# Kernel tuning notes

Measured on AMD Instinct MI355X. Metric: run time of the kernel, lower is better.

## Reference

```python
import jax, jax.numpy as jnp
import numpy as np

N_NODES = 50000
N_EDGES = 800000
IN_FEATS = 128
OUT_FEATS = 128
HEADS = 2
EW_DIMS = 2
NEG_SLOPE = 0.2


def setup_inputs() -> dict:
    key = jax.random.key(0)
    ks = jax.random.split(key, 8)
    feat = jax.random.normal(ks[0], (N_NODES, IN_FEATS), dtype=jnp.float32)
    e_w = jax.random.uniform(ks[1], (N_EDGES, EW_DIMS), dtype=jnp.float32)
    src = jax.random.randint(ks[2], (N_EDGES,), 0, N_NODES)
    dst = jax.random.randint(ks[3], (N_EDGES,), 0, N_NODES)
    # Learned params: per-head fc weight, attn vectors (xavier-ish scale)
    s = 1.0 / np.sqrt(IN_FEATS)
    W = jax.random.normal(ks[4], (HEADS, OUT_FEATS, IN_FEATS), dtype=jnp.float32) * s
    attn_l = jax.random.normal(ks[5], (HEADS, OUT_FEATS), dtype=jnp.float32) * s
    attn_r = jax.random.normal(ks[6], (HEADS, OUT_FEATS), dtype=jnp.float32) * s
    attn_ew = jax.random.normal(ks[7], (HEADS, EW_DIMS), dtype=jnp.float32)
    return {"feat": feat, "e_w": e_w, "src": src, "dst": dst,
            "W": W, "attn_l": attn_l, "attn_r": attn_r, "attn_ew": attn_ew}


def reference(feat, e_w, src, dst, W, attn_l, attn_r, attn_ew):
    N = feat.shape[0]
    # per-head projection: [N, H, O]
    ft = jnp.einsum('nf,hof->nho', feat, W)
    el = jnp.einsum('nho,ho->nh', ft, attn_l)           # [N, H]
    er = jnp.einsum('nho,ho->nh', ft, attn_r)           # [N, H]
    ew = jnp.einsum('ed,hd->eh', e_w, attn_ew)          # [E, H]
    # u_add_v + edge-weight attention + leaky_relu
    e = jax.nn.leaky_relu(el[src] + er[dst] + ew, NEG_SLOPE)  # [E, H]
    # edge_softmax grouped by destination node (numerically stable)
    emax = jax.ops.segment_max(e, dst, num_segments=N)
    emax = jnp.where(jnp.isfinite(emax), emax, 0.0)
    ee = jnp.exp(e - emax[dst])
    denom = jax.ops.segment_sum(ee, dst, num_segments=N)
    a = ee / jnp.where(denom[dst] > 0, denom[dst], 1.0)       # [E, H]
    # u_mul_e / sum aggregation: [N, H, O]
    m = ft[src] * a[:, :, None]
    rst = jax.ops.segment_sum(m, dst, num_segments=N)
    # residual (Identity since in_feats == out_feats) + elu, then cat heads
    rst = jax.nn.elu(rst + feat[:, None, :])
    return rst.reshape(N, -1)
```

## Files before the change

kernel.cpp:

```cpp
#include <hip/hip_runtime.h>
#include <hip/hip_bf16.h>
#include <math.h>

#define NNODES 50000
#define NEDGES 800000
#define INF 128
#define OUTF 128
#define HEADS 2
#define NEG_SLOPE 0.2f

#define CAP 32
#define OVFCAP 32768

__device__ __forceinline__ unsigned short f2bf(float f) {
    unsigned u = __float_as_uint(f);
    unsigned r = (u + 0x7FFFu + ((u >> 16) & 1u)) >> 16;
    return (unsigned short)r;
}
__device__ __forceinline__ float bf2f(unsigned short b) {
    return __uint_as_float((unsigned)b << 16);
}

typedef __attribute__((ext_vector_type(8))) short frag_ab;
typedef __attribute__((ext_vector_type(4))) float frag_cd;
struct us8 { ushort4 a, b; };

#define APITCH 136
#define EPITCH 68

__global__ __launch_bounds__(256) void prep(const float* __restrict__ W,
                                            const float* __restrict__ attn_l,
                                            const float* __restrict__ attn_r,
                                            int* cursor, int* ovfcnt,
                                            unsigned short* __restrict__ Wb,
                                            float* __restrict__ wl, float* __restrict__ wr,
                                            int N) {
    const int b = blockIdx.x, t = threadIdx.x;
    const int i = b * 256 + t;
    if (i < N) cursor[i] = 0;
    if (i == 0) *ovfcnt = 0;
    if (b < 32) {
        int idx = b * 256 + t;
        float4 g = *(const float4*)(W + (size_t)idx * 4);
        ushort4 v; v.x = f2bf(g.x); v.y = f2bf(g.y); v.z = f2bf(g.z); v.w = f2bf(g.w);
        *(ushort4*)(Wb + (size_t)idx * 4) = v;
    } else if (b == 32) {
        int h = t >> 7, f = t & 127;
        float s = 0.f;
#pragma unroll 8
        for (int o = 0; o < 128; ++o)
            s += attn_l[h * 128 + o] * W[(size_t)(h * 128 + o) * 128 + f];
        wl[t] = s;
    } else if (b == 33) {
        int h = t >> 7, f = t & 127;
        float s = 0.f;
#pragma unroll 8
        for (int o = 0; o < 128; ++o)
            s += attn_r[h * 128 + o] * W[(size_t)(h * 128 + o) * 128 + f];
        wr[t] = s;
    }
}

__global__ __launch_bounds__(256) void gemm_mfma(const float* __restrict__ feat,
                                                 const unsigned short* __restrict__ Wb,
                                                 unsigned short* __restrict__ ftb,
                                                 int N) {
    __shared__ unsigned short Asl[64 * APITCH];
    __shared__ unsigned short Bsl[64 * APITCH];
    const int t = threadIdx.x;
    const int n0 = blockIdx.x * 64;
    const int w = t >> 6, lane = t & 63;
    const int m16 = lane & 15, quad = lane >> 4;

#pragma unroll
    for (int i = 0; i < 8; ++i) {
        int q = t + i * 256;
        int r = q >> 5;
        int c4 = q & 31;
        int gn = n0 + r;
        float4 g = (gn < N) ? *(const float4*)(feat + (size_t)gn * INF + c4 * 4)
                            : make_float4(0.f, 0.f, 0.f, 0.f);
        ushort4 v; v.x = f2bf(g.x); v.y = f2bf(g.y); v.z = f2bf(g.z); v.w = f2bf(g.w);
        *(ushort4*)(&Asl[r * APITCH + c4 * 4]) = v;
    }

    const int arow = w * 16 + m16;

    for (int jt = 0; jt < 4; ++jt) {
        __syncthreads();
#pragma unroll
        for (int i = 0; i < 4; ++i) {
            int q = t + i * 256;
            int r = q >> 4;
            int c8 = q & 15;
            us8 v = *(const us8*)(Wb + (size_t)(jt * 64 + r) * 128 + c8 * 8);
            *(us8*)(&Bsl[r * APITCH + c8 * 8]) = v;
        }
        __syncthreads();

        frag_cd acc[4];
#pragma unroll
        for (int nt = 0; nt < 4; ++nt) acc[nt] = frag_cd{0.f, 0.f, 0.f, 0.f};

#pragma unroll
        for (int kc = 0; kc < 4; ++kc) {
            frag_ab af = *(frag_ab*)(&Asl[arow * APITCH + kc * 32 + quad * 8]);
#pragma unroll
            for (int nt = 0; nt < 4; ++nt) {
                frag_ab bf = *(frag_ab*)(&Bsl[(nt * 16 + m16) * APITCH + kc * 32 + quad * 8]);
                acc[nt] = __builtin_amdgcn_mfma_f32_16x16x32_bf16(af, bf, acc[nt], 0, 0, 0);
            }
        }

        __syncthreads();
        unsigned short* ep = &Bsl[w * 16 * EPITCH];
#pragma unroll
        for (int nt = 0; nt < 4; ++nt) {
#pragma unroll
            for (int reg = 0; reg < 4; ++reg)
                ep[(quad * 4 + reg) * EPITCH + nt * 16 + m16] = f2bf(acc[nt][reg]);
        }
        int r = lane >> 2;
        int c = lane & 3;
        us8 v0 = *(us8*)(&ep[r * EPITCH + c * 16]);
        us8 v1 = *(us8*)(&ep[r * EPITCH + c * 16 + 8]);
        int gm = n0 + w * 16 + r;
        if (gm < N) {
            *(us8*)(ftb + (size_t)gm * 256 + jt * 64 + c * 16) = v0;
            *(us8*)(ftb + (size_t)gm * 256 + jt * 64 + c * 16 + 8) = v1;
        }
    }
}

__global__ __launch_bounds__(256) void eler_kernel(const float* __restrict__ feat,
                                                   const float* __restrict__ wl,
                                                   const float* __restrict__ wr,
                                                   float2* __restrict__ el,
                                                   float2* __restrict__ er, int N) {
    __shared__ float swl[256], swr[256];
    const int t = threadIdx.x;
    swl[t] = wl[t];
    swr[t] = wr[t];
    __syncthreads();
    const int w = t >> 6, lane = t & 63;
    const int n = blockIdx.x * 4 + w;
    if (n >= N) return;
    float2 f = *(const float2*)(feat + (size_t)n * INF + lane * 2);
    float l0 = f.x * swl[lane * 2] + f.y * swl[lane * 2 + 1];
    float l1 = f.x * swl[128 + lane * 2] + f.y * swl[128 + lane * 2 + 1];
    float r0 = f.x * swr[lane * 2] + f.y * swr[lane * 2 + 1];
    float r1 = f.x * swr[128 + lane * 2] + f.y * swr[128 + lane * 2 + 1];
#pragma unroll
    for (int m = 1; m < 64; m <<= 1) {
        l0 += __shfl_xor(l0, m, 64);
        l1 += __shfl_xor(l1, m, 64);
        r0 += __shfl_xor(r0, m, 64);
        r1 += __shfl_xor(r1, m, 64);
    }
    if (lane == 0) {
        el[n] = make_float2(l0, l1);
        er[n] = make_float2(r0, r1);
    }
}

__global__ void edge_fused(const float2* __restrict__ el, const float2* __restrict__ er,
                           const float* __restrict__ e_w, const int* __restrict__ src,
                           const int* __restrict__ dst, const float* __restrict__ attn_ew,
                           int* __restrict__ cursor, int* __restrict__ ovfcnt,
                           uint2* __restrict__ edata, float4* __restrict__ ovf,
                           int E) {
    int e = blockIdx.x * 256 + threadIdx.x;
    if (e >= E) return;
    int s = src[e], d = dst[e];
    float2 ew2 = *(const float2*)(e_w + (size_t)e * 2);
    float2 elv = el[s];
    float2 erv = er[d];
    float v0 = elv.x + erv.x + ew2.x * attn_ew[0] + ew2.y * attn_ew[1];
    float v1 = elv.y + erv.y + ew2.x * attn_ew[2] + ew2.y * attn_ew[3];
    v0 = v0 >= 0.f ? v0 : NEG_SLOPE * v0;
    v1 = v1 >= 0.f ? v1 : NEG_SLOPE * v1;
    float ee0 = __expf(v0);
    float ee1 = __expf(v1);
    int pos = atomicAdd(cursor + d, 1);
    if (pos < CAP) {
        unsigned pk = ((unsigned)f2bf(ee1) << 16) | (unsigned)f2bf(ee0);
        edata[(size_t)d * CAP + pos] = make_uint2((unsigned)s, pk);
    } else {
        int o = atomicAdd(ovfcnt, 1);
        if (o < OVFCAP)
            ovf[o] = make_float4(__int_as_float(d), __int_as_float(s), ee0, ee1);
    }
}

__global__ __launch_bounds__(256) void aggregate(const unsigned short* __restrict__ ftb,
                                                 const float* __restrict__ feat,
                                                 const uint2* __restrict__ edata,
                                                 const int* __restrict__ cursor,
                                                 const int* __restrict__ ovfcnt,
                                                 const float4* __restrict__ ovf,
                                                 float* __restrict__ out, int N) {
    const int t = threadIdx.x;
    const int w = t >> 6, l = t & 63;
    const int n = blockIdx.x * 4 + w;
    if (n >= N) return;
    const int c0 = 4 * l;
    const int h = l >> 5;
    const int cnt = cursor[n];
    const int cmain = cnt < CAP ? cnt : CAP;
    const uint2* eb = edata + (size_t)n * CAP;

    uint2 myrec = (l < cmain) ? eb[l] : make_uint2(0u, 0u);

    float4 acc = make_float4(0.f, 0.f, 0.f, 0.f);
    float dn = 0.f;
#pragma unroll 4
    for (int i = 0; i < cmain; ++i) {
        int s = __shfl((int)myrec.x, i, 64);
        unsigned pk = (unsigned)__shfl((int)myrec.y, i, 64);
        float a = __uint_as_float(h ? (pk & 0xFFFF0000u) : (pk << 16));
        dn += a;
        uint2 v = *(const uint2*)(ftb + (size_t)s * 256 + c0);
        acc.x += a * __uint_as_float(v.x << 16);
        acc.y += a * __uint_as_float(v.x & 0xFFFF0000u);
        acc.z += a * __uint_as_float(v.y << 16);
        acc.w += a * __uint_as_float(v.y & 0xFFFF0000u);
    }
    if (cnt > CAP) {
        int no = *ovfcnt; if (no > OVFCAP) no = OVFCAP;
        for (int i = 0; i < no; ++i) {
            float4 ov = ovf[i];
            if (__float_as_int(ov.x) == n) {
                int s = __float_as_int(ov.y);
                float a = h ? ov.w : ov.z;
                dn += a;
                uint2 v = *(const uint2*)(ftb + (size_t)s * 256 + c0);
                acc.x += a * __uint_as_float(v.x << 16);
                acc.y += a * __uint_as_float(v.x & 0xFFFF0000u);
                acc.z += a * __uint_as_float(v.y << 16);
                acc.w += a * __uint_as_float(v.y & 0xFFFF0000u);
            }
        }
    }
    float inv = dn > 0.f ? 1.0f / dn : 0.f;
    float4 f4 = *(const float4*)(feat + (size_t)n * INF + (c0 & 127));
    float4 r;
    r.x = acc.x * inv + f4.x;
    r.y = acc.y * inv + f4.y;
    r.z = acc.z * inv + f4.z;
    r.w = acc.w * inv + f4.w;
    r.x = r.x > 0.f ? r.x : expm1f(r.x);
    r.y = r.y > 0.f ? r.y : expm1f(r.y);
    r.z = r.z > 0.f ? r.z : expm1f(r.z);
    r.w = r.w > 0.f ? r.w : expm1f(r.w);
    *(float4*)(out + (size_t)n * 256 + c0) = r;
}

extern "C" void kernel_launch(void* const* d_in, const int* in_sizes, int n_in,
                              void* d_out, int out_size, void* d_ws, size_t ws_size,
                              hipStream_t stream) {
    const float* feat    = (const float*)d_in[0];
    const float* e_w     = (const float*)d_in[1];
    const int*   src     = (const int*)d_in[2];
    const int*   dst     = (const int*)d_in[3];
    const float* W       = (const float*)d_in[4];
    const float* attn_l  = (const float*)d_in[5];
    const float* attn_r  = (const float*)d_in[6];
    const float* attn_ew = (const float*)d_in[7];
    float* out = (float*)d_out;

    const int N = in_sizes[0] / INF;
    const int E = in_sizes[2];

    unsigned short* ftb = (unsigned short*)d_ws;
    uint2*  edata  = (uint2*)(ftb + (size_t)N * 256);
    float2* el     = (float2*)(edata + (size_t)N * CAP);
    float2* er     = el + N;
    unsigned short* Wb = (unsigned short*)(er + N);
    float*  wl     = (float*)(Wb + 32768);
    float*  wr     = wl + 256;
    float4* ovf    = (float4*)(wr + 256);
    int*    cursor = (int*)(ovf + OVFCAP);
    int*    ovfcnt = cursor + N;

    int pgrid = (N + 255) / 256; if (pgrid < 34) pgrid = 34;
    prep<<<pgrid, 256, 0, stream>>>(W, attn_l, attn_r, cursor, ovfcnt, Wb, wl, wr, N);

    gemm_mfma<<<(N + 63) / 64, 256, 0, stream>>>(feat, Wb, ftb, N);

    eler_kernel<<<(N + 3) / 4, 256, 0, stream>>>(feat, wl, wr, el, er, N);

    edge_fused<<<(E + 255) / 256, 256, 0, stream>>>(el, er, e_w, src, dst, attn_ew,
                                                    cursor, ovfcnt, edata, ovf, E);

    aggregate<<<(N + 3) / 4, 256, 0, stream>>>(ftb, feat, edata, cursor, ovfcnt, ovf, out, N);
}
```

Baseline: 248.2 us.

## Bin edges by destination and source bucket, aggregate several nodes per wave

Edges are now binned by destination node and by source-index bucket, with eight slots per bin instead of one 32-slot list per node. The aggregation kernel gives each wave 13 destination nodes and walks the source buckets in order, so concurrent gathers of the bf16 feature rows hit a narrower source range and should get better cache reuse. In exchange the cursor array grows eightfold and the edge buffer doubles. Each wave also holds 13 accumulators, which raises register pressure. Small per-bin capacity sends more edges to the linearly scanned overflow list, and the fixed inner loop wastes lanes on empty slots.

```diff
diff --git a/kernel.cpp b/kernel.cpp
--- a/kernel.cpp
+++ b/kernel.cpp
@@ -9,17 +9,17 @@
 #define HEADS 2
 #define NEG_SLOPE 0.2f
 
-#define CAP 32
+#define SUBCAP 8
+#define NBINS_PER_NODE 8
+#define BUCKET_SHIFT 13
 #define OVFCAP 32768
+#define NPW 13
 
 __device__ __forceinline__ unsigned short f2bf(float f) {
     unsigned u = __float_as_uint(f);
     unsigned r = (u + 0x7FFFu + ((u >> 16) & 1u)) >> 16;
     return (unsigned short)r;
 }
-__device__ __forceinline__ float bf2f(unsigned short b) {
-    return __uint_as_float((unsigned)b << 16);
-}
 
 typedef __attribute__((ext_vector_type(8))) short frag_ab;
 typedef __attribute__((ext_vector_type(4))) float frag_cd;
@@ -31,13 +31,13 @@
 __global__ __launch_bounds__(256) void prep(const float* __restrict__ W,
                                             const float* __restrict__ attn_l,
                                             const float* __restrict__ attn_r,
-                                            int* cursor, int* ovfcnt,
+                                            int* cursor2, int* ovfcnt,
                                             unsigned short* __restrict__ Wb,
                                             float* __restrict__ wl, float* __restrict__ wr,
-                                            int N) {
+                                            int NC) {
     const int b = blockIdx.x, t = threadIdx.x;
     const int i = b * 256 + t;
-    if (i < N) cursor[i] = 0;
+    if (i < NC) cursor2[i] = 0;
     if (i == 0) *ovfcnt = 0;
     if (b < 32) {
         int idx = b * 256 + t;
@@ -166,8 +166,8 @@
 __global__ void edge_fused(const float2* __restrict__ el, const float2* __restrict__ er,
                            const float* __restrict__ e_w, const int* __restrict__ src,
                            const int* __restrict__ dst, const float* __restrict__ attn_ew,
-                           int* __restrict__ cursor, int* __restrict__ ovfcnt,
-                           uint2* __restrict__ edata, float4* __restrict__ ovf,
+                           int* __restrict__ cursor2, int* __restrict__ ovfcnt,
+                           uint2* __restrict__ edata2, float4* __restrict__ ovf,
                            int E) {
     int e = blockIdx.x * 256 + threadIdx.x;
     if (e >= E) return;
@@ -181,10 +181,11 @@
     v1 = v1 >= 0.f ? v1 : NEG_SLOPE * v1;
     float ee0 = __expf(v0);
     float ee1 = __expf(v1);
-    int pos = atomicAdd(cursor + d, 1);
-    if (pos < CAP) {
+    int bin = d * NBINS_PER_NODE + (s >> BUCKET_SHIFT);
+    int pos = atomicAdd(cursor2 + bin, 1);
+    if (pos < SUBCAP) {
         unsigned pk = ((unsigned)f2bf(ee1) << 16) | (unsigned)f2bf(ee0);
-        edata[(size_t)d * CAP + pos] = make_uint2((unsigned)s, pk);
+        edata2[(size_t)bin * SUBCAP + pos] = make_uint2((unsigned)s, pk);
     } else {
         int o = atomicAdd(ovfcnt, 1);
         if (o < OVFCAP)
@@ -192,67 +193,100 @@
     }
 }
 
-__global__ __launch_bounds__(256) void aggregate(const unsigned short* __restrict__ ftb,
-                                                 const float* __restrict__ feat,
-                                                 const uint2* __restrict__ edata,
-                                                 const int* __restrict__ cursor,
-                                                 const int* __restrict__ ovfcnt,
-                                                 const float4* __restrict__ ovf,
-                                                 float* __restrict__ out, int N) {
+__global__ __launch_bounds__(256, 4) void aggregate_p(const unsigned short* __restrict__ ftb,
+                                                      const float* __restrict__ feat,
+                                                      const uint2* __restrict__ edata2,
+                                                      const int* __restrict__ cursor2,
+                                                      const int* __restrict__ ovfcnt,
+                                                      const float4* __restrict__ ovf,
+                                                      float* __restrict__ out,
+                                                      int N, int nbuck) {
     const int t = threadIdx.x;
-    const int w = t >> 6, l = t & 63;
-    const int n = blockIdx.x * 4 + w;
-    if (n >= N) return;
+    const int g = blockIdx.x * 4 + (t >> 6);
+    const int l = t & 63;
+    const int nb = g * NPW;
+    if (nb >= N) return;
+    int kmax = N - nb; if (kmax > NPW) kmax = NPW;
     const int c0 = 4 * l;
     const int h = l >> 5;
-    const int cnt = cursor[n];
-    const int cmain = cnt < CAP ? cnt : CAP;
-    const uint2* eb = edata + (size_t)n * CAP;
-
-    uint2 myrec = (l < cmain) ? eb[l] : make_uint2(0u, 0u);
-
-    float4 acc = make_float4(0.f, 0.f, 0.f, 0.f);
-    float dn = 0.f;
-#pragma unroll 4
-    for (int i = 0; i < cmain; ++i) {
-        int s = __shfl((int)myrec.x, i, 64);
-        unsigned pk = (unsigned)__shfl((int)myrec.y, i, 64);
-        float a = __uint_as_float(h ? (pk & 0xFFFF0000u) : (pk << 16));
-        dn += a;
-        uint2 v = *(const uint2*)(ftb + (size_t)s * 256 + c0);
-        acc.x += a * __uint_as_float(v.x << 16);
-        acc.y += a * __uint_as_float(v.x & 0xFFFF0000u);
-        acc.z += a * __uint_as_float(v.y << 16);
-        acc.w += a * __uint_as_float(v.y & 0xFFFF0000u);
-    }
-    if (cnt > CAP) {
-        int no = *ovfcnt; if (no > OVFCAP) no = OVFCAP;
+    const int ln_node = l >> 3, ln_slot = l & 7;
+
+    float4 acc[NPW];
+    float dn[NPW];
+#pragma unroll
+    for (int k = 0; k < NPW; ++k) { acc[k] = make_float4(0.f,0.f,0.f,0.f); dn[k] = 0.f; }
+    int cmax_l = 0;
+
+    for (int b = 0; b < nbuck; ++b) {
+        int cnt_l = 0;
+        if (l < kmax) cnt_l = cursor2[(nb + l) * NBINS_PER_NODE + b];
+        cmax_l = cnt_l > cmax_l ? cnt_l : cmax_l;
+        uint2 r0 = make_uint2(0u, 0u), r1 = make_uint2(0u, 0u);
+        if (ln_node < kmax)
+            r0 = edata2[((size_t)(nb + ln_node) * NBINS_PER_NODE + b) * SUBCAP + ln_slot];
+        if (8 + ln_node < kmax)
+            r1 = edata2[((size_t)(nb + 8 + ln_node) * NBINS_PER_NODE + b) * SUBCAP + ln_slot];
+#pragma unroll
+        for (int k = 0; k < NPW; ++k) {
+            if (k >= kmax) break;
+            int cnt = __shfl(cnt_l, k, 64);
+            if (cnt > SUBCAP) cnt = SUBCAP;
+            uint2 rr = (k < 8) ? r0 : r1;
+            int baseln = (k & 7) * 8;
+#pragma unroll
+            for (int i = 0; i < SUBCAP; ++i) {
+                if (i < cnt) {
+                    int s = __shfl((int)rr.x, baseln + i, 64);
+                    unsigned pk = (unsigned)__shfl((int)rr.y, baseln + i, 64);
+                    float a = __uint_as_float(h ? (pk & 0xFFFF0000u) : (pk << 16));
+                    dn[k] += a;
+                    uint2 v = *(const uint2*)(ftb + (size_t)s * 256 + c0);
+                    acc[k].x += a * __uint_as_float(v.x << 16);
+                    acc[k].y += a * __uint_as_float(v.x & 0xFFFF0000u);
+                    acc[k].z += a * __uint_as_float(v.y << 16);
+                    acc[k].w += a * __uint_as_float(v.y & 0xFFFF0000u);
+                }
+            }
+        }
+    }
+
+    int no = *ovfcnt; if (no > OVFCAP) no = OVFCAP;
+#pragma unroll
+    for (int k = 0; k < NPW; ++k) {
+        if (k >= kmax) break;
+        if (__shfl(cmax_l, k, 64) <= SUBCAP) continue;
         for (int i = 0; i < no; ++i) {
             float4 ov = ovf[i];
-            if (__float_as_int(ov.x) == n) {
+            if (__float_as_int(ov.x) == nb + k) {
                 int s = __float_as_int(ov.y);
                 float a = h ? ov.w : ov.z;
-                dn += a;
+                dn[k] += a;
                 uint2 v = *(const uint2*)(ftb + (size_t)s * 256 + c0);
-                acc.x += a * __uint_as_float(v.x << 16);
-                acc.y += a * __uint_as_float(v.x & 0xFFFF0000u);
-                acc.z += a * __uint_as_float(v.y << 16);
-                acc.w += a * __uint_as_float(v.y & 0xFFFF0000u);
+                acc[k].x += a * __uint_as_float(v.x << 16);
+                acc[k].y += a * __uint_as_float(v.x & 0xFFFF0000u);
+                acc[k].z += a * __uint_as_float(v.y << 16);
+                acc[k].w += a * __uint_as_float(v.y & 0xFFFF0000u);
             }
         }
     }
-    float inv = dn > 0.f ? 1.0f / dn : 0.f;
-    float4 f4 = *(const float4*)(feat + (size_t)n * INF + (c0 & 127));
-    float4 r;
-    r.x = acc.x * inv + f4.x;
-    r.y = acc.y * inv + f4.y;
-    r.z = acc.z * inv + f4.z;
-    r.w = acc.w * inv + f4.w;
-    r.x = r.x > 0.f ? r.x : expm1f(r.x);
-    r.y = r.y > 0.f ? r.y : expm1f(r.y);
-    r.z = r.z > 0.f ? r.z : expm1f(r.z);
-    r.w = r.w > 0.f ? r.w : expm1f(r.w);
-    *(float4*)(out + (size_t)n * 256 + c0) = r;
+
+#pragma unroll
+    for (int k = 0; k < NPW; ++k) {
+        if (k >= kmax) break;
+        int n = nb + k;
+        float inv = dn[k] > 0.f ? 1.0f / dn[k] : 0.f;
+        float4 f4 = *(const float4*)(feat + (size_t)n * INF + (c0 & 127));
+        float4 r;
+        r.x = acc[k].x * inv + f4.x;
+        r.y = acc[k].y * inv + f4.y;
+        r.z = acc[k].z * inv + f4.z;
+        r.w = acc[k].w * inv + f4.w;
+        r.x = r.x > 0.f ? r.x : expm1f(r.x);
+        r.y = r.y > 0.f ? r.y : expm1f(r.y);
+        r.z = r.z > 0.f ? r.z : expm1f(r.z);
+        r.w = r.w > 0.f ? r.w : expm1f(r.w);
+        *(float4*)(out + (size_t)n * 256 + c0) = r;
+    }
 }
 
 extern "C" void kernel_launch(void* const* d_in, const int* in_sizes, int n_in,
@@ -272,25 +306,30 @@
     const int E = in_sizes[2];
 
     unsigned short* ftb = (unsigned short*)d_ws;
-    uint2*  edata  = (uint2*)(ftb + (size_t)N * 256);
-    float2* el     = (float2*)(edata + (size_t)N * CAP);
+    uint2*  edata2 = (uint2*)(ftb + (size_t)N * 256);
+    float2* el     = (float2*)(edata2 + (size_t)N * NBINS_PER_NODE * SUBCAP);
     float2* er     = el + N;
     unsigned short* Wb = (unsigned short*)(er + N);
     float*  wl     = (float*)(Wb + 32768);
     float*  wr     = wl + 256;
     float4* ovf    = (float4*)(wr + 256);
-    int*    cursor = (int*)(ovf + OVFCAP);
-    int*    ovfcnt = cursor + N;
-
-    int pgrid = (N + 255) / 256; if (pgrid < 34) pgrid = 34;
-    prep<<<pgrid, 256, 0, stream>>>(W, attn_l, attn_r, cursor, ovfcnt, Wb, wl, wr, N);
+    int*    cursor2= (int*)(ovf + OVFCAP);
+    int*    ovfcnt = cursor2 + (size_t)N * NBINS_PER_NODE;
+
+    const int NC = N * NBINS_PER_NODE;
+    int pgrid = (NC + 255) / 256; if (pgrid < 34) pgrid = 34;
+    prep<<<pgrid, 256, 0, stream>>>(W, attn_l, attn_r, cursor2, ovfcnt, Wb, wl, wr, NC);
 
     gemm_mfma<<<(N + 63) / 64, 256, 0, stream>>>(feat, Wb, ftb, N);
 
     eler_kernel<<<(N + 3) / 4, 256, 0, stream>>>(feat, wl, wr, el, er, N);
 
     edge_fused<<<(E + 255) / 256, 256, 0, stream>>>(el, er, e_w, src, dst, attn_ew,
-                                                    cursor, ovfcnt, edata, ovf, E);
-
-    aggregate<<<(N + 3) / 4, 256, 0, stream>>>(ftb, feat, edata, cursor, ovfcnt, ovf, out, N);
-}
+                                                    cursor2, ovfcnt, edata2, ovf, E);
+
+    const int nbuck = ((N - 1) >> BUCKET_SHIFT) + 1;
+    const int nwaves = (N + NPW - 1) / NPW;
+    const int ablocks = (nwaves + 3) / 4;
+    aggregate_p<<<ablocks, 256, 0, stream>>>(ftb, feat, edata2, cursor2, ovfcnt, ovf,
+                                             out, N, nbuck);
+}
```

Result: slower. 551.9 us (+122.4%).
